# Kernel tuning notes

Hardware: AMD Instinct MI355X
Metric: run time of the kernel (lower is better)

## Reference

```python
import jax, jax.numpy as jnp
import numpy as np

N_NODES = 200000
N_EDGES = 1600000
NUM_GRAPHS = 2000
VOCAB = 10000
D = 64
NUM_CLS = 2


def setup_inputs() -> dict:
    key = jax.random.key(0)
    ks = jax.random.split(key, 12)
    x = jax.random.randint(ks[0], (N_NODES,), 0, VOCAB, dtype=jnp.int32)
    edge_index = jax.random.randint(ks[1], (2, N_EDGES), 0, N_NODES, dtype=jnp.int32)
    edge_type = jax.random.randint(ks[2], (N_EDGES,), 0, 8, dtype=jnp.int32)
    batch = jnp.sort(jax.random.randint(ks[3], (N_NODES,), 0, NUM_GRAPHS, dtype=jnp.int32))
    embed_table = jax.random.normal(ks[4], (VOCAB, D), dtype=jnp.float32) * 0.02
    embed_table = embed_table.at[0].set(0.0)  # padding_idx=0
    W1 = jax.random.normal(ks[5], (D, D), dtype=jnp.float32) * (1.0 / np.sqrt(D))
    b1 = jnp.zeros((D,), dtype=jnp.float32)
    W2 = jax.random.normal(ks[6], (D, D), dtype=jnp.float32) * (1.0 / np.sqrt(D))
    b2 = jnp.zeros((D,), dtype=jnp.float32)
    Wlin = jax.random.normal(ks[7], (D, NUM_CLS), dtype=jnp.float32) * (1.0 / np.sqrt(D))
    blin = jnp.zeros((NUM_CLS,), dtype=jnp.float32)
    return {"x": x, "edge_index": edge_index, "edge_type": edge_type, "batch": batch,
            "embed_table": embed_table, "W1": W1, "b1": b1, "W2": W2, "b2": b2,
            "Wlin": Wlin, "blin": blin}


def reference(x, edge_index, edge_type, batch, embed_table, W1, b1, W2, b2, Wlin, blin):
    n = x.shape[0]
    # GCN normalization with self-loops (PyG GCNConv default, edge weight = 1)
    loops = jnp.arange(n, dtype=edge_index.dtype)
    src = jnp.concatenate([edge_index[0], loops])
    dst = jnp.concatenate([edge_index[1], loops])
    deg = jax.ops.segment_sum(jnp.ones_like(src, dtype=jnp.float32), dst, num_segments=n)
    dinv = jax.lax.rsqrt(deg)  # deg >= 1 due to self-loops
    norm = (dinv[src] * dinv[dst])[:, None]  # [E+N, 1]

    def gcn(h, W, b):
        h = h @ W  # transform first (small GEMM)
        agg = jax.ops.segment_sum(norm * h[src], dst, num_segments=n)
        return agg + b

    h = embed_table[x]                      # [N, D] embedding lookup
    h = jax.nn.relu(gcn(h, W1, b1))
    h = jax.nn.relu(gcn(h, W2, b2))
    # global mean pool over graphs
    sums = jax.ops.segment_sum(h, batch, num_segments=NUM_GRAPHS)
    cnts = jax.ops.segment_sum(jnp.ones((n,), dtype=h.dtype), batch, num_segments=NUM_GRAPHS)
    g = sums / jnp.maximum(cnts, 1.0)[:, None]
    return g @ Wlin + blin
```

## Files before the change

kernel.cpp:

```cpp
#include <hip/hip_runtime.h>
#include <hip/hip_fp16.h>


#define DD 64
#define BKT 256
#define MAXK 1024
#define NBLK 256
#define SLACK 772

typedef _Float16 half8_t __attribute__((ext_vector_type(8)));
typedef float float4_t __attribute__((ext_vector_type(4)));
union F4H8 { float4 f; half8_t h; };
union H8   { float4 f; __half2 h[4]; };

static __device__ __forceinline__ void atomAddF(float* p, float v) {
    unsafeAtomicAdd(p, v);
}

__global__ __launch_bounds__(256) void bin_count_kernel(
        const int* __restrict__ dst, int E, int CH,
        int* __restrict__ hist, int K,
        const float2* __restrict__ table2, __half2* __restrict__ th2, int n2,
        const float* __restrict__ W1, const float* __restrict__ W2,
        __half* __restrict__ w1t, __half* __restrict__ w2t) {
    __shared__ int lh[MAXK];
    int tid = threadIdx.x;
    for (int i = tid; i < K; i += 256) lh[i] = 0;
    __syncthreads();
    int stride = gridDim.x * 256;
    for (int i = blockIdx.x * 256 + tid; i < n2; i += stride)
        th2[i] = __float22half2_rn(table2[i]);
    for (int i = blockIdx.x * 256 + tid; i < DD * DD; i += stride) {
        int n = i >> 6, k = i & 63;
        w1t[i] = __float2half(W1[k * DD + n]);
        w2t[i] = __float2half(W2[k * DD + n]);
    }
    int e0 = blockIdx.x * CH;
    int e1 = min(E, e0 + CH);
    for (int e = e0 + tid; e < e1; e += 256)
        atomicAdd(&lh[((unsigned)dst[e]) >> 8], 1);
    __syncthreads();
    for (int b = tid; b < K; b += 256)
        hist[blockIdx.x * MAXK + b] = lh[b];
}

__global__ __launch_bounds__(256) void totals_kernel(
        const int* __restrict__ hist, int* __restrict__ bts,
        float* __restrict__ outacc, int K, int G2) {
    int g0 = blockIdx.x * 256 + threadIdx.x;
    int stride = gridDim.x * 256;
    for (int i = g0; i < G2; i += stride) outacc[i] = 0.f;
    for (int b = g0; b < K; b += stride) {
        int s = 0;
        for (int blk = 0; blk < NBLK; ++blk) s += hist[blk * MAXK + b];
        bts[b] = s;
    }
}

__global__ __launch_bounds__(256) void scan_bb_kernel(
        const int* __restrict__ bts, int* __restrict__ bb, int K, int E) {
    __shared__ int part[256];
    int tid = threadIdx.x;
    int CH2 = (K + 255) / 256;
    int base = tid * CH2;
    int s = 0;
    for (int i = 0; i < CH2; ++i) {
        int idx = base + i;
        if (idx < K) s += bts[idx];
    }
    part[tid] = s;
    __syncthreads();
    if (tid < 64) {
        int carry = 0;
        for (int c = 0; c < 4; ++c) {
            int orig = part[c * 64 + tid];
            int v = orig;
            #pragma unroll
            for (int off = 1; off < 64; off <<= 1) {
                int t = __shfl_up(v, off);
                if (tid >= off) v += t;
            }
            int tot = __shfl(v, 63);
            part[c * 64 + tid] = v - orig + carry;
            carry += tot;
        }
    }
    __syncthreads();
    int run = part[tid];
    for (int i = 0; i < CH2; ++i) {
        int idx = base + i;
        if (idx < K) {
            bb[idx] = run;
            run += bts[idx];
        }
    }
    if (tid == 0) bb[K] = E;
}

__global__ __launch_bounds__(256) void scanB_kernel(
        const int* __restrict__ hist, const int* __restrict__ bb,
        int* __restrict__ cur, int K) {
    int b = blockIdx.x * 256 + threadIdx.x;
    if (b >= K) return;
    int run = bb[b];
    for (int blk = 0; blk < NBLK; ++blk) {
        cur[blk * MAXK + b] = run;
        run += hist[blk * MAXK + b];
    }
}

__global__ __launch_bounds__(256) void fill_kernel(
        const int* __restrict__ src, const int* __restrict__ dst, int E, int CH,
        const int* __restrict__ cur, int* __restrict__ pairbuf, int K) {
    __shared__ int lcur[MAXK];
    int tid = threadIdx.x;
    for (int b = tid; b < K; b += 256)
        lcur[b] = cur[blockIdx.x * MAXK + b];
    __syncthreads();
    int e0 = blockIdx.x * CH;
    int e1 = min(E, e0 + CH);
    for (int e = e0 + tid; e < e1; e += 256) {
        int s = src[e], d = dst[e];
        int pos = atomicAdd(&lcur[((unsigned)d) >> 8], 1);
        pairbuf[pos] = s | ((d & 255) << 24);
    }
}

__global__ __launch_bounds__(256) void build_csr_kernel(
        const int* __restrict__ pairbuf, const int* __restrict__ bnd,
        const int* __restrict__ x, int2* __restrict__ rowinfo,
        float2* __restrict__ xd,
        int* __restrict__ csr_src, __half* __restrict__ g1h, int N) {
    __shared__ int cnt[256], basel[256], curl[256];
    int tid = threadIdx.x;
    int b = blockIdx.x;
    int node0 = b << 8;
    cnt[tid] = 0;
    __syncthreads();
    int bb0 = bnd[b], bb1 = bnd[b + 1];
    for (int i = bb0 + tid; i < bb1; i += 256)
        atomicAdd(&cnt[((unsigned)pairbuf[i]) >> 24], 1);
    __syncthreads();
    int c  = cnt[tid];
    int pc = (c + 3) & ~3;
    {
        __syncthreads();
        basel[tid] = pc;
        __syncthreads();
        if (tid < 64) {
            int carry = 0;
            for (int cc = 0; cc < 4; ++cc) {
                int orig = basel[cc * 64 + tid];
                int v = orig;
                #pragma unroll
                for (int off = 1; off < 64; off <<= 1) {
                    int t = __shfl_up(v, off);
                    if (tid >= off) v += t;
                }
                int tot = __shfl(v, 63);
                cnt[cc * 64 + tid] = v - orig + carry;
                carry += tot;
            }
        }
        __syncthreads();
    }
    int cb0 = ((bb0 + 3) & ~3) + SLACK * b;
    int node = node0 + tid;
    int myBase = cb0 + cnt[tid];
    curl[tid] = myBase;
    if (node < N) {
        rowinfo[node] = make_int2(myBase, pc);
        xd[node] = make_float2(rsqrtf((float)c + 1.0f), __int_as_float(x[node]));
        for (int t = c; t < pc; ++t) csr_src[myBase + t] = N;
    } else if (node == N) {
        xd[N] = make_float2(0.0f, __int_as_float(0));
        float2* z = (float2*)(g1h + (size_t)N * DD);
        for (int t = 0; t < DD / 4; ++t) z[t] = make_float2(0.f, 0.f);
    }
    __syncthreads();
    for (int i = bb0 + tid; i < bb1; i += 256) {
        int pk = pairbuf[i];
        int pos = atomicAdd(&curl[((unsigned)pk) >> 24], 1);
        csr_src[pos] = pk & 0x00FFFFFF;
    }
}

__global__ __launch_bounds__(256, 8) void layer1_kernel(
        const int2* __restrict__ rowinfo,
        const int* __restrict__ csr_src, const float2* __restrict__ xd,
        const float4* __restrict__ th4, const __half* __restrict__ wt,
        const float* __restrict__ bias, __half* __restrict__ g1h, int N) {
    __shared__ float4 Hs4[32 * 9];
    __shared__ float dvs[32];
    int row0 = blockIdx.x * 32;
    int tid = threadIdx.x;
    int node_l = tid >> 3, j3 = tid & 7;
    int node = row0 + node_l;
    H8 acc0, acc1;
    acc0.f = make_float4(0.f, 0.f, 0.f, 0.f);
    acc1.f = acc0.f;
    if (node < N) {
        float2 sxd = xd[node];
        float di = sxd.x;
        if (j3 == 0) dvs[node_l] = di;
        __half2 dh = __float2half2_rn(di);
        H8 tv; tv.f = th4[(size_t)__float_as_int(sxd.y) * 8 + j3];
        acc0.h[0] = __hmul2(dh, tv.h[0]); acc0.h[1] = __hmul2(dh, tv.h[1]);
        acc0.h[2] = __hmul2(dh, tv.h[2]); acc0.h[3] = __hmul2(dh, tv.h[3]);
        int2 ri = rowinfo[node];
        const int4* cs = (const int4*)(csr_src + ri.x);
        int nq = ri.y >> 2;
        for (int q = 0; q < nq; ++q) {
            int4 s4 = cs[q];
            float2 pa = xd[s4.x], pb = xd[s4.y], pc_ = xd[s4.z], pd = xd[s4.w];
            __half2 w0 = __float2half2_rn(pa.x);
            __half2 w1 = __float2half2_rn(pb.x);
            __half2 w2 = __float2half2_rn(pc_.x);
            __half2 w3 = __float2half2_rn(pd.x);
            H8 u0, u1, u2, u3;
            u0.f = th4[(size_t)__float_as_int(pa.y)  * 8 + j3];
            u1.f = th4[(size_t)__float_as_int(pb.y)  * 8 + j3];
            u2.f = th4[(size_t)__float_as_int(pc_.y) * 8 + j3];
            u3.f = th4[(size_t)__float_as_int(pd.y)  * 8 + j3];
            #pragma unroll
            for (int t = 0; t < 4; ++t) {
                acc0.h[t] = __hfma2(w0, u0.h[t], acc0.h[t]);
                acc1.h[t] = __hfma2(w1, u1.h[t], acc1.h[t]);
                acc0.h[t] = __hfma2(w2, u2.h[t], acc0.h[t]);
                acc1.h[t] = __hfma2(w3, u3.h[t], acc1.h[t]);
            }
        }
        #pragma unroll
        for (int t = 0; t < 4; ++t)
            acc0.h[t] = __hmul2(dh, __hadd2(acc0.h[t], acc1.h[t]));
    }
    Hs4[node_l * 9 + j3] = acc0.f;
    __syncthreads();

    int wave = tid >> 6, lane = tid & 63;
    int m = lane & 15, quad = lane >> 4;
    int ncol = wave * 16 + m;
    F4H8 b0, b1;
    const float4* WT4 = (const float4*)wt;
    b0.f = WT4[ncol * 8 + quad];
    b1.f = WT4[ncol * 8 + 4 + quad];
    float bb_ = bias[ncol];
    #pragma unroll
    for (int t = 0; t < 2; ++t) {
        F4H8 a0, a1;
        a0.f = Hs4[(t * 16 + m) * 9 + quad];
        a1.f = Hs4[(t * 16 + m) * 9 + 4 + quad];
        float4_t acc = {0.f, 0.f, 0.f, 0.f};
        acc = __builtin_amdgcn_mfma_f32_16x16x32_f16(a0.h, b0.h, acc, 0, 0, 0);
        acc = __builtin_amdgcn_mfma_f32_16x16x32_f16(a1.h, b1.h, acc, 0, 0, 0);
        #pragma unroll
        for (int reg = 0; reg < 4; ++reg) {
            int row = t * 16 + quad * 4 + reg;
            int grow = row0 + row;
            if (grow < N) {
                float h = fmaxf(acc[reg] + bb_, 0.0f);
                g1h[(size_t)grow * DD + ncol] = __float2half(dvs[row] * h);
            }
        }
    }
}

__global__ __launch_bounds__(256, 8) void layer2_pool_kernel(
        const int2* __restrict__ rowinfo,
        const int* __restrict__ csr_src, const float2* __restrict__ xd,
        const float4* __restrict__ g1h4, const __half* __restrict__ wt,
        const float* __restrict__ bias, const int* __restrict__ batch,
        const float* __restrict__ Wlin, float* __restrict__ outacc, int N) {
    __shared__ float4 Hs4[32 * 9];
    __shared__ float lp0[128], lp1[128];
    __shared__ float p0s[32], p1s[32];
    __shared__ int   bat[32];
    int row0 = blockIdx.x * 32;
    int tid = threadIdx.x;
    int node_l = tid >> 3, j3 = tid & 7;
    int node = row0 + node_l;
    H8 acc0, acc1;
    acc0.f = make_float4(0.f, 0.f, 0.f, 0.f);
    acc1.f = acc0.f;
    if (node < N) {
        float di = xd[node].x;
        acc0.f = g1h4[(size_t)node * 8 + j3];
        int2 ri = rowinfo[node];
        const int4* cs = (const int4*)(csr_src + ri.x);
        int nq = ri.y >> 2;
        for (int q = 0; q < nq; ++q) {
            int4 s4 = cs[q];
            H8 u0, u1, u2, u3;
            u0.f = g1h4[(size_t)s4.x * 8 + j3];
            u1.f = g1h4[(size_t)s4.y * 8 + j3];
            u2.f = g1h4[(size_t)s4.z * 8 + j3];
            u3.f = g1h4[(size_t)s4.w * 8 + j3];
            #pragma unroll
            for (int t = 0; t < 4; ++t) {
                acc0.h[t] = __hadd2(acc0.h[t], u0.h[t]);
                acc1.h[t] = __hadd2(acc1.h[t], u1.h[t]);
                acc0.h[t] = __hadd2(acc0.h[t], u2.h[t]);
                acc1.h[t] = __hadd2(acc1.h[t], u3.h[t]);
            }
        }
        __half2 dih = __float2half2_rn(di);
        #pragma unroll
        for (int t = 0; t < 4; ++t)
            acc0.h[t] = __hmul2(dih, __hadd2(acc0.h[t], acc1.h[t]));
    }
    Hs4[node_l * 9 + j3] = acc0.f;
    __syncthreads();

    int wave = tid >> 6, lane = tid & 63;
    int m = lane & 15, quad = lane >> 4;
    int ncol = wave * 16 + m;
    F4H8 b0, b1;
    const float4* WT4 = (const float4*)wt;
    b0.f = WT4[ncol * 8 + quad];
    b1.f = WT4[ncol * 8 + 4 + quad];
    float bb_  = bias[ncol];
    float wl0 = Wlin[ncol * 2 + 0];
    float wl1 = Wlin[ncol * 2 + 1];
    #pragma unroll
    for (int t = 0; t < 2; ++t) {
        F4H8 a0, a1;
        a0.f = Hs4[(t * 16 + m) * 9 + quad];
        a1.f = Hs4[(t * 16 + m) * 9 + 4 + quad];
        float4_t acc = {0.f, 0.f, 0.f, 0.f};
        acc = __builtin_amdgcn_mfma_f32_16x16x32_f16(a0.h, b0.h, acc, 0, 0, 0);
        acc = __builtin_amdgcn_mfma_f32_16x16x32_f16(a1.h, b1.h, acc, 0, 0, 0);
        #pragma unroll
        for (int reg = 0; reg < 4; ++reg) {
            int row = t * 16 + quad * 4 + reg;
            int grow = row0 + row;
            float h = (grow < N) ? fmaxf(acc[reg] + bb_, 0.0f) : 0.0f;
            float p0 = h * wl0;
            float p1 = h * wl1;
            #pragma unroll
            for (int off = 8; off >= 1; off >>= 1) {
                p0 += __shfl_xor(p0, off);
                p1 += __shfl_xor(p1, off);
            }
            if (m == 0) {
                lp0[wave * 32 + row] = p0;
                lp1[wave * 32 + row] = p1;
            }
        }
    }
    __syncthreads();
    if (tid < 32) {
        int grow = row0 + tid;
        p0s[tid] = lp0[tid] + lp0[32 + tid] + lp0[64 + tid] + lp0[96 + tid];
        p1s[tid] = lp1[tid] + lp1[32 + tid] + lp1[64 + tid] + lp1[96 + tid];
        bat[tid] = (grow < N) ? batch[grow] : -1;
    }
    __syncthreads();
    if (tid < 32) {
        int bg = bat[tid];
        bool head = (bg >= 0) && (tid == 0 || bat[tid - 1] != bg);
        if (head) {
            float s0 = 0.f, s1 = 0.f;
            for (int k = tid; k < 32 && bat[k] == bg; ++k) {
                s0 += p0s[k];
                s1 += p1s[k];
            }
            atomAddF(&outacc[bg * 2 + 0], s0);
            atomAddF(&outacc[bg * 2 + 1], s1);
        }
    }
}

__global__ void final_kernel(const float* __restrict__ outacc,
                             const int* __restrict__ batch,
                             const float* __restrict__ blin,
                             float* __restrict__ out, int G, int N) {
    int t = blockIdx.x * blockDim.x + threadIdx.x;
    if (t >= G * 2) return;
    int g = t >> 1, c = t & 1;
    int lo = 0, hi = N;
    while (lo < hi) { int m = (lo + hi) >> 1; if (batch[m] < g) lo = m + 1; else hi = m; }
    int lo2 = lo, hi2 = N;
    while (lo2 < hi2) { int m = (lo2 + hi2) >> 1; if (batch[m] < g + 1) lo2 = m + 1; else hi2 = m; }
    float cnt = (float)(lo2 - lo);
    out[t] = outacc[t] / fmaxf(cnt, 1.0f) + blin[c];
}

extern "C" void kernel_launch(void* const* d_in, const int* in_sizes, int n_in,
                              void* d_out, int out_size, void* d_ws, size_t ws_size,
                              hipStream_t stream) {
    const int*   x      = (const int*)d_in[0];
    const int*   ei     = (const int*)d_in[1];
    const int*   batch  = (const int*)d_in[3];
    const float* table  = (const float*)d_in[4];
    const float* W1     = (const float*)d_in[5];
    const float* b1     = (const float*)d_in[6];
    const float* W2     = (const float*)d_in[7];
    const float* b2     = (const float*)d_in[8];
    const float* Wlin   = (const float*)d_in[9];
    const float* blin   = (const float*)d_in[10];
    float* out = (float*)d_out;

    const int N = in_sizes[0];
    const int E = in_sizes[2];
    const int G = out_size / 2;
    const int TBL = in_sizes[4];

    const int* src = ei;
    const int* dst = ei + E;

    const int K = (N + BKT - 1) / BKT;
    const int M = NBLK * MAXK;
    const int CH = (E + NBLK - 1) / NBLK;
    const int CSRSZ = E + SLACK * K + 64;

    __half* g1h     = (__half*)d_ws;
    __half* th      = g1h + (size_t)(N + 1) * DD;
    __half* w1t     = th + TBL;
    __half* w2t     = w1t + DD * DD;
    int*    pairbuf = (int*)(w2t + DD * DD);
    int*    csr_src = pairbuf + E;
    int2*   rowinfo = (int2*)(csr_src + CSRSZ);
    float2* xd      = (float2*)(rowinfo + N);
    float*  outacc  = (float*)(xd + N + 1);
    int*    bb      = (int*)(outacc + 2 * G);
    int*    bts     = bb + K + 1;
    int*    hist    = bts + K;
    int*    cur     = hist + M;

    const int BT = 256;

    bin_count_kernel<<<NBLK, BT, 0, stream>>>(dst, E, CH, hist, K,
                                              (const float2*)table,
                                              (__half2*)th, TBL / 2,
                                              W1, W2, w1t, w2t);
    totals_kernel<<<16, BT, 0, stream>>>(hist, bts, outacc, K, 2 * G);
    scan_bb_kernel<<<1, BT, 0, stream>>>(bts, bb, K, E);
    scanB_kernel<<<(K + BT - 1) / BT, BT, 0, stream>>>(hist, bb, cur, K);
    fill_kernel<<<NBLK, BT, 0, stream>>>(src, dst, E, CH, cur, pairbuf, K);
    build_csr_kernel<<<K, BT, 0, stream>>>(pairbuf, bb, x, rowinfo, xd,
                                           csr_src, g1h, N);

    int gRow = (N + 31) / 32;
    layer1_kernel<<<gRow, BT, 0, stream>>>(rowinfo, csr_src, xd,
                                           (const float4*)th, w1t, b1, g1h, N);
    layer2_pool_kernel<<<gRow, BT, 0, stream>>>(rowinfo, csr_src, xd,
                                                (const float4*)g1h, w2t, b2,
                                                batch, Wlin, outacc, N);
    final_kernel<<<(G * 2 + BT - 1) / BT, BT, 0, stream>>>(outacc, batch, blin,
                                                           out, G, N);
}
```

Measured before the change: 240.3 us.

## Parallelize per-bucket scan across a wavefront and unroll gather loops deeper

scanB now gives each bucket a full 64-lane wavefront: every lane loads four block histogram entries and a shuffle-based prefix scan replaces the serial 256-step loop per thread. The layer1 and layer2 gather loops handle two int4 index groups per iteration with four independent accumulators, so more gathers are in flight at once. Launch bounds drop from 8 to 6 waves per SIMD to leave room for the extra registers. The trade-off is lower occupancy for more memory-level parallelism per thread.

```diff
diff --git a/kernel.cpp b/kernel.cpp
--- a/kernel.cpp
+++ b/kernel.cpp
@@ -100,13 +100,26 @@
 __global__ __launch_bounds__(256) void scanB_kernel(
         const int* __restrict__ hist, const int* __restrict__ bb,
         int* __restrict__ cur, int K) {
-    int b = blockIdx.x * 256 + threadIdx.x;
-    if (b >= K) return;
-    int run = bb[b];
-    for (int blk = 0; blk < NBLK; ++blk) {
-        cur[blk * MAXK + b] = run;
-        run += hist[blk * MAXK + b];
-    }
+    int wid = (blockIdx.x * 256 + threadIdx.x) >> 6;
+    int lane = threadIdx.x & 63;
+    if (wid >= K) return;
+    int b = wid;
+    int v0 = hist[(lane * 4 + 0) * MAXK + b];
+    int v1 = hist[(lane * 4 + 1) * MAXK + b];
+    int v2 = hist[(lane * 4 + 2) * MAXK + b];
+    int v3 = hist[(lane * 4 + 3) * MAXK + b];
+    int sum = v0 + v1 + v2 + v3;
+    int pref = sum;
+    #pragma unroll
+    for (int off = 1; off < 64; off <<= 1) {
+        int t = __shfl_up(pref, off);
+        if (lane >= off) pref += t;
+    }
+    int run = bb[b] + pref - sum;
+    cur[(lane * 4 + 0) * MAXK + b] = run; run += v0;
+    cur[(lane * 4 + 1) * MAXK + b] = run; run += v1;
+    cur[(lane * 4 + 2) * MAXK + b] = run; run += v2;
+    cur[(lane * 4 + 3) * MAXK + b] = run;
 }
 
 __global__ __launch_bounds__(256) void fill_kernel(
@@ -185,7 +198,7 @@
     }
 }
 
-__global__ __launch_bounds__(256, 8) void layer1_kernel(
+__global__ __launch_bounds__(256, 6) void layer1_kernel(
         const int2* __restrict__ rowinfo,
         const int* __restrict__ csr_src, const float2* __restrict__ xd,
         const float4* __restrict__ th4, const __half* __restrict__ wt,
@@ -196,43 +209,73 @@
     int tid = threadIdx.x;
     int node_l = tid >> 3, j3 = tid & 7;
     int node = row0 + node_l;
-    H8 acc0, acc1;
+    H8 acc0, acc1, acc2, acc3;
     acc0.f = make_float4(0.f, 0.f, 0.f, 0.f);
-    acc1.f = acc0.f;
+    acc1.f = acc0.f; acc2.f = acc0.f; acc3.f = acc0.f;
+    __half2 dh = __float2half2_rn(0.f);
     if (node < N) {
         float2 sxd = xd[node];
         float di = sxd.x;
         if (j3 == 0) dvs[node_l] = di;
-        __half2 dh = __float2half2_rn(di);
+        dh = __float2half2_rn(di);
         H8 tv; tv.f = th4[(size_t)__float_as_int(sxd.y) * 8 + j3];
         acc0.h[0] = __hmul2(dh, tv.h[0]); acc0.h[1] = __hmul2(dh, tv.h[1]);
         acc0.h[2] = __hmul2(dh, tv.h[2]); acc0.h[3] = __hmul2(dh, tv.h[3]);
         int2 ri = rowinfo[node];
         const int4* cs = (const int4*)(csr_src + ri.x);
         int nq = ri.y >> 2;
-        for (int q = 0; q < nq; ++q) {
-            int4 s4 = cs[q];
-            float2 pa = xd[s4.x], pb = xd[s4.y], pc_ = xd[s4.z], pd = xd[s4.w];
-            __half2 w0 = __float2half2_rn(pa.x);
-            __half2 w1 = __float2half2_rn(pb.x);
-            __half2 w2 = __float2half2_rn(pc_.x);
-            __half2 w3 = __float2half2_rn(pd.x);
+        int q = 0;
+        for (; q + 1 < nq; q += 2) {
+            int4 sA = cs[q], sB = cs[q + 1];
+            float2 pa = xd[sA.x], pb = xd[sA.y], pc_ = xd[sA.z], pd = xd[sA.w];
+            float2 pe = xd[sB.x], pf = xd[sB.y], pg = xd[sB.z], ph = xd[sB.w];
+            H8 u0, u1, u2, u3, u4, u5, u6, u7;
+            u0.f = th4[(size_t)__float_as_int(pa.y)  * 8 + j3];
+            u1.f = th4[(size_t)__float_as_int(pb.y)  * 8 + j3];
+            u2.f = th4[(size_t)__float_as_int(pc_.y) * 8 + j3];
+            u3.f = th4[(size_t)__float_as_int(pd.y)  * 8 + j3];
+            u4.f = th4[(size_t)__float_as_int(pe.y)  * 8 + j3];
+            u5.f = th4[(size_t)__float_as_int(pf.y)  * 8 + j3];
+            u6.f = th4[(size_t)__float_as_int(pg.y)  * 8 + j3];
+            u7.f = th4[(size_t)__float_as_int(ph.y)  * 8 + j3];
+            __half2 w0 = __float2half2_rn(pa.x), w1 = __float2half2_rn(pb.x);
+            __half2 w2 = __float2half2_rn(pc_.x), w3 = __float2half2_rn(pd.x);
+            __half2 w4 = __float2half2_rn(pe.x), w5 = __float2half2_rn(pf.x);
+            __half2 w6 = __float2half2_rn(pg.x), w7 = __float2half2_rn(ph.x);
+            #pragma unroll
+            for (int t = 0; t < 4; ++t) {
+                acc0.h[t] = __hfma2(w0, u0.h[t], acc0.h[t]);
+                acc1.h[t] = __hfma2(w1, u1.h[t], acc1.h[t]);
+                acc2.h[t] = __hfma2(w2, u2.h[t], acc2.h[t]);
+                acc3.h[t] = __hfma2(w3, u3.h[t], acc3.h[t]);
+                acc0.h[t] = __hfma2(w4, u4.h[t], acc0.h[t]);
+                acc1.h[t] = __hfma2(w5, u5.h[t], acc1.h[t]);
+                acc2.h[t] = __hfma2(w6, u6.h[t], acc2.h[t]);
+                acc3.h[t] = __hfma2(w7, u7.h[t], acc3.h[t]);
+            }
+        }
+        if (q < nq) {
+            int4 sA = cs[q];
+            float2 pa = xd[sA.x], pb = xd[sA.y], pc_ = xd[sA.z], pd = xd[sA.w];
             H8 u0, u1, u2, u3;
             u0.f = th4[(size_t)__float_as_int(pa.y)  * 8 + j3];
             u1.f = th4[(size_t)__float_as_int(pb.y)  * 8 + j3];
             u2.f = th4[(size_t)__float_as_int(pc_.y) * 8 + j3];
             u3.f = th4[(size_t)__float_as_int(pd.y)  * 8 + j3];
+            __half2 w0 = __float2half2_rn(pa.x), w1 = __float2half2_rn(pb.x);
+            __half2 w2 = __float2half2_rn(pc_.x), w3 = __float2half2_rn(pd.x);
             #pragma unroll
             for (int t = 0; t < 4; ++t) {
                 acc0.h[t] = __hfma2(w0, u0.h[t], acc0.h[t]);
                 acc1.h[t] = __hfma2(w1, u1.h[t], acc1.h[t]);
-                acc0.h[t] = __hfma2(w2, u2.h[t], acc0.h[t]);
-                acc1.h[t] = __hfma2(w3, u3.h[t], acc1.h[t]);
+                acc2.h[t] = __hfma2(w2, u2.h[t], acc2.h[t]);
+                acc3.h[t] = __hfma2(w3, u3.h[t], acc3.h[t]);
             }
         }
         #pragma unroll
         for (int t = 0; t < 4; ++t)
-            acc0.h[t] = __hmul2(dh, __hadd2(acc0.h[t], acc1.h[t]));
+            acc0.h[t] = __hmul2(dh, __hadd2(__hadd2(acc0.h[t], acc1.h[t]),
+                                            __hadd2(acc2.h[t], acc3.h[t])));
     }
     Hs4[node_l * 9 + j3] = acc0.f;
     __syncthreads();
@@ -265,7 +308,7 @@
     }
 }
 
-__global__ __launch_bounds__(256, 8) void layer2_pool_kernel(
+__global__ __launch_bounds__(256, 6) void layer2_pool_kernel(
         const int2* __restrict__ rowinfo,
         const int* __restrict__ csr_src, const float2* __restrict__ xd,
         const float4* __restrict__ g1h4, const __half* __restrict__ wt,
@@ -279,34 +322,59 @@
     int tid = threadIdx.x;
     int node_l = tid >> 3, j3 = tid & 7;
     int node = row0 + node_l;
-    H8 acc0, acc1;
+    H8 acc0, acc1, acc2, acc3;
     acc0.f = make_float4(0.f, 0.f, 0.f, 0.f);
-    acc1.f = acc0.f;
+    acc1.f = acc0.f; acc2.f = acc0.f; acc3.f = acc0.f;
     if (node < N) {
         float di = xd[node].x;
         acc0.f = g1h4[(size_t)node * 8 + j3];
         int2 ri = rowinfo[node];
         const int4* cs = (const int4*)(csr_src + ri.x);
         int nq = ri.y >> 2;
-        for (int q = 0; q < nq; ++q) {
-            int4 s4 = cs[q];
-            H8 u0, u1, u2, u3;
-            u0.f = g1h4[(size_t)s4.x * 8 + j3];
-            u1.f = g1h4[(size_t)s4.y * 8 + j3];
-            u2.f = g1h4[(size_t)s4.z * 8 + j3];
-            u3.f = g1h4[(size_t)s4.w * 8 + j3];
+        int q = 0;
+        for (; q + 1 < nq; q += 2) {
+            int4 sA = cs[q], sB = cs[q + 1];
+            H8 u0, u1, u2, u3, u4, u5, u6, u7;
+            u0.f = g1h4[(size_t)sA.x * 8 + j3];
+            u1.f = g1h4[(size_t)sA.y * 8 + j3];
+            u2.f = g1h4[(size_t)sA.z * 8 + j3];
+            u3.f = g1h4[(size_t)sA.w * 8 + j3];
+            u4.f = g1h4[(size_t)sB.x * 8 + j3];
+            u5.f = g1h4[(size_t)sB.y * 8 + j3];
+            u6.f = g1h4[(size_t)sB.z * 8 + j3];
+            u7.f = g1h4[(size_t)sB.w * 8 + j3];
             #pragma unroll
             for (int t = 0; t < 4; ++t) {
                 acc0.h[t] = __hadd2(acc0.h[t], u0.h[t]);
                 acc1.h[t] = __hadd2(acc1.h[t], u1.h[t]);
-                acc0.h[t] = __hadd2(acc0.h[t], u2.h[t]);
-                acc1.h[t] = __hadd2(acc1.h[t], u3.h[t]);
+                acc2.h[t] = __hadd2(acc2.h[t], u2.h[t]);
+                acc3.h[t] = __hadd2(acc3.h[t], u3.h[t]);
+                acc0.h[t] = __hadd2(acc0.h[t], u4.h[t]);
+                acc1.h[t] = __hadd2(acc1.h[t], u5.h[t]);
+                acc2.h[t] = __hadd2(acc2.h[t], u6.h[t]);
+                acc3.h[t] = __hadd2(acc3.h[t], u7.h[t]);
+            }
+        }
+        if (q < nq) {
+            int4 sA = cs[q];
+            H8 u0, u1, u2, u3;
+            u0.f = g1h4[(size_t)sA.x * 8 + j3];
+            u1.f = g1h4[(size_t)sA.y * 8 + j3];
+            u2.f = g1h4[(size_t)sA.z * 8 + j3];
+            u3.f = g1h4[(size_t)sA.w * 8 + j3];
+            #pragma unroll
+            for (int t = 0; t < 4; ++t) {
+                acc0.h[t] = __hadd2(acc0.h[t], u0.h[t]);
+                acc1.h[t] = __hadd2(acc1.h[t], u1.h[t]);
+                acc2.h[t] = __hadd2(acc2.h[t], u2.h[t]);
+                acc3.h[t] = __hadd2(acc3.h[t], u3.h[t]);
             }
         }
         __half2 dih = __float2half2_rn(di);
         #pragma unroll
         for (int t = 0; t < 4; ++t)
-            acc0.h[t] = __hmul2(dih, __hadd2(acc0.h[t], acc1.h[t]));
+            acc0.h[t] = __hmul2(dih, __hadd2(__hadd2(acc0.h[t], acc1.h[t]),
+                                             __hadd2(acc2.h[t], acc3.h[t])));
     }
     Hs4[node_l * 9 + j3] = acc0.f;
     __syncthreads();
@@ -435,7 +503,7 @@
                                               W1, W2, w1t, w2t);
     totals_kernel<<<16, BT, 0, stream>>>(hist, bts, outacc, K, 2 * G);
     scan_bb_kernel<<<1, BT, 0, stream>>>(bts, bb, K, E);
-    scanB_kernel<<<(K + BT - 1) / BT, BT, 0, stream>>>(hist, bb, cur, K);
+    scanB_kernel<<<(K * 64 + BT - 1) / BT, BT, 0, stream>>>(hist, bb, cur, K);
     fill_kernel<<<NBLK, BT, 0, stream>>>(src, dst, E, CH, cur, pairbuf, K);
     build_csr_kernel<<<K, BT, 0, stream>>>(pairbuf, bb, x, rowinfo, xd,
                                            csr_src, g1h, N);
```

Measured after the change: 240.2 us. About the same (-0.0%).
